# Optimization experiments

Hardware: AMD Instinct MI355X
Metric: run time of the kernel (lower is better)

## Reference

```python
import jax, jax.numpy as jnp
import numpy as np

EPS = 1e-5
NUM_HEAD = 8
HEAD_DIM = 64
SCALE = HEAD_DIM ** -0.5


def setup_inputs() -> dict:
    key = jax.random.key(0)
    ks = jax.random.split(key, 3)
    b, n, dim = 4, 2048, 512
    inner = NUM_HEAD * HEAD_DIM  # 512
    x = jax.random.normal(ks[0], (b, n, dim), dtype=jnp.float32)
    ln_w = jnp.ones((dim,), jnp.float32)
    ln_b = jnp.zeros((dim,), jnp.float32)
    qkv_w = jax.random.normal(ks[1], (3 * inner, dim), jnp.float32) * (dim ** -0.5)
    qkv_b = jnp.zeros((3 * inner,), jnp.float32)
    out_w = jax.random.normal(ks[2], (dim, inner), jnp.float32) * (inner ** -0.5)
    out_b = jnp.zeros((dim,), jnp.float32)
    return {"x": x, "ln_w": ln_w, "ln_b": ln_b, "qkv_w": qkv_w,
            "qkv_b": qkv_b, "out_w": out_w, "out_b": out_b}


def reference(x, ln_w, ln_b, qkv_w, qkv_b, out_w, out_b):
    b, n, dim = x.shape
    # Pre-norm LayerNorm
    mu = jnp.mean(x, axis=-1, keepdims=True)
    var = jnp.mean(jnp.square(x - mu), axis=-1, keepdims=True)
    xn = (x - mu) * jax.lax.rsqrt(var + EPS) * ln_w + ln_b
    # QKV projection (torch Linear: y = x @ W.T + b)
    qkv = xn @ qkv_w.T + qkv_b  # [b, n, 3*inner]
    q, k, v = jnp.split(qkv, 3, axis=-1)
    def heads(t):  # [b, n, inner] -> [b, h, n, d]
        return t.reshape(b, n, NUM_HEAD, HEAD_DIM).transpose(0, 2, 1, 3)
    q, k, v = heads(q), heads(k), heads(v)
    # Naive full attention (materializes [b, h, n, n])
    dots = jnp.einsum('bhqd,bhkd->bhqk', q, k) * SCALE
    attn = jax.nn.softmax(dots, axis=-1)
    o = jnp.einsum('bhqk,bhkd->bhqd', attn, v)
    o = o.transpose(0, 2, 1, 3).reshape(b, n, NUM_HEAD * HEAD_DIM)
    return o @ out_w.T + out_b
```

## Files before the change

kernel.cpp:

```cpp
#include <hip/hip_runtime.h>

typedef __attribute__((ext_vector_type(8))) short bf16x8;
typedef __attribute__((ext_vector_type(4))) float floatx4;
typedef __attribute__((ext_vector_type(16))) float floatx16;
typedef __attribute__((ext_vector_type(4))) unsigned int uintx4;

#define B_    4
#define N_    2048
#define DIM_  512
#define NH_   8
#define HD_   64
#define SCALE_ 0.125f
#define SL2E_ (0.125f * 1.44269504f)

__device__ __forceinline__ unsigned short f32_to_bf16(float f) {
    return (unsigned short)((__float_as_uint(f) + 0x8000u) >> 16);
}

__device__ __forceinline__ float bf16_to_f32(unsigned short u) {
    return __uint_as_float(((unsigned int)u) << 16);
}

__device__ __forceinline__ floatx4 mfma16(bf16x8 a, bf16x8 b, floatx4 c) {
    return __builtin_amdgcn_mfma_f32_16x16x32_bf16(a, b, c, 0, 0, 0);
}

__device__ __forceinline__ floatx16 mfma32(bf16x8 a, bf16x8 b, floatx16 c) {
    return __builtin_amdgcn_mfma_f32_32x32x16_bf16(a, b, c, 0, 0, 0);
}

__device__ __forceinline__ floatx4 fzero4() {
    floatx4 z = {0.f, 0.f, 0.f, 0.f};
    return z;
}

__device__ __forceinline__ floatx16 fzero16() {
    floatx16 z;
#pragma unroll
    for (int i = 0; i < 16; i++) z[i] = 0.f;
    return z;
}

__device__ __forceinline__ unsigned int cvt_pk_bf16(float lo, float hi) {
    unsigned int r;
    asm("v_cvt_pk_bf16_f32 %0, %1, %2" : "=v"(r) : "v"(lo), "v"(hi));
    return r;
}

__device__ __forceinline__ void async16(const unsigned short* g, unsigned short* l) {
    __builtin_amdgcn_global_load_lds((const __attribute__((address_space(1))) void*)g,
                                     (__attribute__((address_space(3))) void*)l,
                                     16, 0, 0);
}

__global__ __launch_bounds__(256) void ln_kernel(const float* __restrict__ x,
                                                 const float* __restrict__ w,
                                                 const float* __restrict__ b,
                                                 unsigned short* __restrict__ xn) {
    int wv = threadIdx.x >> 6;
    int lane = threadIdx.x & 63;
    int row = blockIdx.x * 4 + wv;
    const float4* xr = (const float4*)(x + (size_t)row * DIM_);
    float4 v0 = xr[lane * 2];
    float4 v1 = xr[lane * 2 + 1];
    float s  = (v0.x + v0.y + v0.z + v0.w) + (v1.x + v1.y + v1.z + v1.w);
    float sq = v0.x*v0.x + v0.y*v0.y + v0.z*v0.z + v0.w*v0.w +
               v1.x*v1.x + v1.y*v1.y + v1.z*v1.z + v1.w*v1.w;
#pragma unroll
    for (int off = 1; off < 64; off <<= 1) {
        s  += __shfl_xor(s, off, 64);
        sq += __shfl_xor(sq, off, 64);
    }
    float mu   = s * (1.f / DIM_);
    float var  = sq * (1.f / DIM_) - mu * mu;
    float rstd = rsqrtf(var + 1e-5f);
    float4 w0 = ((const float4*)w)[lane * 2];
    float4 w1 = ((const float4*)w)[lane * 2 + 1];
    float4 b0 = ((const float4*)b)[lane * 2];
    float4 b1 = ((const float4*)b)[lane * 2 + 1];
    float y[8];
    y[0] = (v0.x - mu) * rstd * w0.x + b0.x;
    y[1] = (v0.y - mu) * rstd * w0.y + b0.y;
    y[2] = (v0.z - mu) * rstd * w0.z + b0.z;
    y[3] = (v0.w - mu) * rstd * w0.w + b0.w;
    y[4] = (v1.x - mu) * rstd * w1.x + b1.x;
    y[5] = (v1.y - mu) * rstd * w1.y + b1.y;
    y[6] = (v1.z - mu) * rstd * w1.z + b1.z;
    y[7] = (v1.w - mu) * rstd * w1.w + b1.w;
    uint4 pk;
    pk.x = (unsigned int)f32_to_bf16(y[0]) | ((unsigned int)f32_to_bf16(y[1]) << 16);
    pk.y = (unsigned int)f32_to_bf16(y[2]) | ((unsigned int)f32_to_bf16(y[3]) << 16);
    pk.z = (unsigned int)f32_to_bf16(y[4]) | ((unsigned int)f32_to_bf16(y[5]) << 16);
    pk.w = (unsigned int)f32_to_bf16(y[6]) | ((unsigned int)f32_to_bf16(y[7]) << 16);
    ((uint4*)(xn + (size_t)row * DIM_))[lane] = pk;
}

__global__ __launch_bounds__(256) void cvt_kernel(const float* __restrict__ srcA, int na,
                                                  const float* __restrict__ srcB, int nb,
                                                  unsigned short* __restrict__ dstA,
                                                  unsigned short* __restrict__ dstB) {
    int idx = blockIdx.x * 256 + threadIdx.x;
    if (idx < na)            dstA[idx] = f32_to_bf16(srcA[idx]);
    else if (idx < na + nb)  dstB[idx - na] = f32_to_bf16(srcB[idx - na]);
}

#define GEMM_CORE512(A_, B_ptr, am0, bn0)                                           \
    __shared__ unsigned short Alds[2][128][32];                                     \
    __shared__ unsigned short Blds[2][128][32];                                     \
    int tid = threadIdx.x, lane = tid & 63, wid = tid >> 6;                         \
    int l15 = lane & 15, quad = lane >> 4;                                          \
    int wmloc = (wid >> 1) * 32, wnloc = (wid & 1) * 64;                            \
    int sr = lane >> 2;                                                             \
    int sc = (lane & 3) * 8;                                                        \
    int srow0 = 16 * wid;                                                           \
    floatx4 acc[2][4];                                                              \
    _Pragma("unroll")                                                               \
    for (int i = 0; i < 2; i++)                                                     \
        _Pragma("unroll")                                                           \
        for (int j = 0; j < 4; j++) acc[i][j] = fzero4();                           \
    int buf = 0;                                                                    \
    async16(A_ + (size_t)(am0 + srow0 + sr) * DIM_ + sc, &Alds[0][srow0][0]);       \
    async16(B_ptr + (size_t)(bn0 + srow0 + sr) * DIM_ + sc, &Blds[0][srow0][0]);    \
    __syncthreads();                                                                \
    for (int t = 0; t < 16; t++) {                                                  \
        if (t < 15) {                                                               \
            int k0 = (t + 1) * 32;                                                  \
            async16(A_ + (size_t)(am0 + srow0 + sr) * DIM_ + k0 + sc,               \
                    &Alds[buf ^ 1][srow0][0]);                                      \
            async16(B_ptr + (size_t)(bn0 + srow0 + sr) * DIM_ + k0 + sc,            \
                    &Blds[buf ^ 1][srow0][0]);                                      \
        }                                                                           \
        bf16x8 av[2], bv[4];                                                        \
        _Pragma("unroll")                                                           \
        for (int i = 0; i < 2; i++)                                                 \
            av[i] = *(const bf16x8*)(&Alds[buf][wmloc + 16 * i + l15][quad * 8]);   \
        _Pragma("unroll")                                                           \
        for (int j = 0; j < 4; j++)                                                 \
            bv[j] = *(const bf16x8*)(&Blds[buf][wnloc + 16 * j + l15][quad * 8]);   \
        _Pragma("unroll")                                                           \
        for (int i = 0; i < 2; i++)                                                 \
            _Pragma("unroll")                                                       \
            for (int j = 0; j < 4; j++)                                             \
                acc[i][j] = mfma16(av[i], bv[j], acc[i][j]);                        \
        __syncthreads();                                                            \
        buf ^= 1;                                                                   \
    }

__global__ __launch_bounds__(512, 6) void qkv_gemm(const unsigned short* __restrict__ A,
                                                   const unsigned short* __restrict__ Bw,
                                                   const float* __restrict__ bias,
                                                   unsigned short* __restrict__ Qh,
                                                   unsigned short* __restrict__ Kh,
                                                   unsigned short* __restrict__ Vt) {
    int am0 = blockIdx.x * 128, bn0 = blockIdx.y * 128;
    GEMM_CORE512(A, Bw, am0, bn0)

    if (bn0 >= 1024) {
        unsigned short* sc_ = &Alds[0][0][0] + wid * (16 * 40);
        int m0 = am0 + wmloc;
        int bidx = m0 >> 11;
        int t0 = m0 & 2047;
#pragma unroll
        for (int j = 0; j < 4; j++) {
            float bias_n = bias[bn0 + wnloc + 16 * j + l15];
#pragma unroll
            for (int i = 0; i < 2; i++)
#pragma unroll
                for (int r = 0; r < 4; r++)
                    sc_[l15 * 40 + 16 * i + quad * 4 + r] =
                        f32_to_bf16(acc[i][j][r] + bias_n);
            int nr = lane >> 2;
            int rem = (bn0 - 1024) + wnloc + 16 * j + nr;
            int head = rem >> 6, d = rem & 63;
            bf16x8 vv = *(const bf16x8*)(sc_ + nr * 40 + (lane & 3) * 8);
            *(bf16x8*)(Vt + ((size_t)(bidx * NH_ + head) * HD_ + d) * N_ +
                       t0 + (lane & 3) * 8) = vv;
        }
    } else {
#pragma unroll
        for (int i = 0; i < 2; i++) {
#pragma unroll
            for (int j = 0; j < 4; j++) {
                int n = bn0 + wnloc + 16 * j + l15;
                float bias_n = bias[n];
                int which = n >> 9;
                int rem = n & 511;
                int head = rem >> 6;
                int d = rem & 63;
#pragma unroll
                for (int r = 0; r < 4; r++) {
                    int m = am0 + wmloc + 16 * i + quad * 4 + r;
                    int b = m >> 11;
                    int t = m & 2047;
                    float val = acc[i][j][r] + bias_n;
                    if (which == 0) {
                        Qh[((size_t)(b * NH_ + head) * N_ + t) * HD_ + d] =
                            f32_to_bf16(val * SL2E_);
                    } else {
                        Kh[((size_t)(b * NH_ + head) * N_ + t) * HD_ + d] =
                            f32_to_bf16(val);
                    }
                }
            }
        }
    }
}

__global__ __launch_bounds__(256, 4) void out_gemm_fused(const unsigned short* __restrict__ Opart,
                                                         const float* __restrict__ lpart,
                                                         const unsigned short* __restrict__ Bw,
                                                         const float* __restrict__ bias,
                                                         float* __restrict__ out) {
    __shared__ unsigned short Alds[2][64][36];
    __shared__ unsigned short Blds[2][128][32];
    int tid = threadIdx.x, lane = tid & 63, wid = tid >> 6;
    int l15 = lane & 15, quad = lane >> 4;
    int wmloc = (wid >> 1) * 32, wnloc = (wid & 1) * 64;
    int am0 = blockIdx.x * 64, bn0 = blockIdx.y * 128;

    int arow = tid >> 2;
    int ac8 = (tid & 3) * 8;
    int token = am0 + arow;
    int bb = token >> 11;
    const size_t LSTR = (size_t)B_ * NH_ * N_;
    const size_t OSTR = (size_t)B_ * N_ * DIM_;
    const unsigned short* arow0 = Opart + (size_t)token * DIM_;
    const unsigned short* arow1 = arow0 + OSTR;

    int sr = lane >> 2;
    int sc = (lane & 3) * 8;

    floatx4 acc[2][4];
#pragma unroll
    for (int i = 0; i < 2; i++)
#pragma unroll
        for (int j = 0; j < 4; j++) acc[i][j] = fzero4();

#define STAGE_A(BUF, T)                                                         \
    {                                                                           \
        int k0 = (T) * 32;                                                      \
        int head = k0 >> 6;                                                     \
        size_t li = (size_t)(bb * NH_ + head) * N_ + (token & 2047);            \
        float l1 = lpart[li];                                                   \
        float l2 = lpart[LSTR + li];                                            \
        float inv = 1.f / (l1 + l2);                                            \
        float w1 = l1 * inv, w2 = l2 * inv;                                     \
        bf16x8 o0 = *(const bf16x8*)(arow0 + k0 + ac8);                         \
        bf16x8 o1 = *(const bf16x8*)(arow1 + k0 + ac8);                         \
        bf16x8 pk;                                                              \
        _Pragma("unroll")                                                       \
        for (int e = 0; e < 8; e++)                                             \
            pk[e] = (short)f32_to_bf16(                                         \
                w1 * bf16_to_f32((unsigned short)o0[e]) +                       \
                w2 * bf16_to_f32((unsigned short)o1[e]));                       \
        *(bf16x8*)(&Alds[BUF][arow][ac8]) = pk;                                 \
    }

#define STAGE_B(BUF, T)                                                         \
    {                                                                           \
        int k0 = (T) * 32;                                                      \
        _Pragma("unroll")                                                       \
        for (int i = 0; i < 2; i++) {                                           \
            int r0 = 32 * wid + 16 * i;                                         \
            async16(Bw + (size_t)(bn0 + r0 + sr) * DIM_ + k0 + sc,              \
                    &Blds[BUF][r0][0]);                                         \
        }                                                                       \
    }

    STAGE_B(0, 0)
    STAGE_A(0, 0)
    __syncthreads();
    int buf = 0;
    for (int t = 0; t < 16; t++) {
        if (t < 15) {
            STAGE_B(buf ^ 1, t + 1)
            STAGE_A(buf ^ 1, t + 1)
        }
        bf16x8 av[2], bv[4];
#pragma unroll
        for (int i = 0; i < 2; i++)
            av[i] = *(const bf16x8*)(&Alds[buf][wmloc + 16 * i + l15][quad * 8]);
#pragma unroll
        for (int j = 0; j < 4; j++)
            bv[j] = *(const bf16x8*)(&Blds[buf][wnloc + 16 * j + l15][quad * 8]);
#pragma unroll
        for (int i = 0; i < 2; i++)
#pragma unroll
            for (int j = 0; j < 4; j++)
                acc[i][j] = mfma16(av[i], bv[j], acc[i][j]);
        __syncthreads();
        buf ^= 1;
    }
#undef STAGE_A
#undef STAGE_B

#pragma unroll
    for (int i = 0; i < 2; i++) {
#pragma unroll
        for (int j = 0; j < 4; j++) {
            int n = bn0 + wnloc + 16 * j + l15;
            float bias_n = bias[n];
#pragma unroll
            for (int r = 0; r < 4; r++) {
                int m = am0 + wmloc + 16 * i + quad * 4 + r;
                out[(size_t)m * DIM_ + n] = acc[i][j][r] + bias_n;
            }
        }
    }
}

__global__ __launch_bounds__(256, 4) void attn_kernel(const unsigned short* __restrict__ Qh,
                                                      const unsigned short* __restrict__ Kh,
                                                      const unsigned short* __restrict__ Vtg,
                                                      unsigned short* __restrict__ Opart,
                                                      float* __restrict__ lpart) {
    int bh = blockIdx.y;
    int b = bh >> 3, head = bh & 7;
    int qt = blockIdx.x;
    int split = blockIdx.z;
    int kv0 = split << 10;
    int tid = threadIdx.x, lane = tid & 63, w = tid >> 6;
    int l31 = lane & 31, hi = lane >> 5;
    int xr = l31 & 7;

    const unsigned short* Qp = Qh + (size_t)bh * N_ * HD_;
    const unsigned short* Kg = Kh + (size_t)bh * N_ * HD_;
    const unsigned short* Vg = Vtg + (size_t)bh * HD_ * N_;

    int q0 = qt * 128 + w * 32;

    bf16x8 aQ[4];
    {
        const unsigned short* qrow = Qp + (size_t)(q0 + l31) * HD_ + hi * 8;
#pragma unroll
        for (int t = 0; t < 4; t++)
            aQ[t] = *(const bf16x8*)(qrow + 16 * t);
    }

    __shared__ unsigned short KV[2][2][64][64];
    __shared__ float l_sm[4][32];

    int srow = lane >> 3;
    int scol = ((lane & 7) ^ srow) * 8;

    const char* ptc[4];
#pragma unroll
    for (int t = 0; t < 4; t++)
        ptc[t] = (const char*)&KV[0][0][l31][(((2 * t + hi) ^ xr) * 8)];

    const unsigned short* kSrc = Kg + (size_t)(kv0 + 16 * w + srow) * HD_ + scol;
    const unsigned short* vSrc = Vg + (size_t)(16 * w + srow) * N_ + kv0 + scol;

#define STAGE_KV(BUF, IT)                                                       \
    {                                                                           \
        _Pragma("unroll")                                                       \
        for (int i = 0; i < 2; i++) {                                           \
            int r0 = 16 * w + 8 * i;                                            \
            async16(kSrc + (size_t)(IT) * 64 * HD_ + i * 8 * HD_,               \
                    &KV[BUF][0][r0][0]);                                        \
            async16(vSrc + (size_t)(IT) * 64 + i * 8 * N_,                      \
                    &KV[BUF][1][r0][0]);                                        \
        }                                                                       \
    }

    floatx16 of[2];
    of[0] = fzero16();
    of[1] = fzero16();
    float lsA = 0.f, lsB = 0.f;

#define COMPUTE(BUF)                                                            \
    {                                                                           \
        bf16x8 pa[4];                                                           \
        _Pragma("unroll")                                                       \
        for (int tau = 0; tau < 2; tau++) {                                     \
            bf16x8 kf[4];                                                       \
            _Pragma("unroll")                                                   \
            for (int t = 0; t < 4; t++)                                         \
                kf[t] = *(const bf16x8*)(ptc[t] + (BUF) * 16384 + tau * 4096);  \
            floatx16 acc = fzero16();                                           \
            __builtin_amdgcn_s_setprio(1);                                      \
            _Pragma("unroll")                                                   \
            for (int t = 0; t < 4; t++)                                         \
                acc = mfma32(kf[t], aQ[t], acc);                                \
            __builtin_amdgcn_s_setprio(0);                                      \
            float p[16];                                                        \
            _Pragma("unroll")                                                   \
            for (int r = 0; r < 16; r += 2) {                                   \
                p[r]     = __builtin_amdgcn_exp2f(acc[r]);                      \
                p[r + 1] = __builtin_amdgcn_exp2f(acc[r + 1]);                  \
                lsA += p[r];                                                    \
                lsB += p[r + 1];                                                \
            }                                                                   \
            unsigned int a0 = cvt_pk_bf16(p[0], p[1]);                          \
            unsigned int b0 = cvt_pk_bf16(p[4], p[5]);                          \
            unsigned int a1 = cvt_pk_bf16(p[2], p[3]);                          \
            unsigned int b1 = cvt_pk_bf16(p[6], p[7]);                          \
            unsigned int a2 = cvt_pk_bf16(p[8], p[9]);                          \
            unsigned int b2 = cvt_pk_bf16(p[12], p[13]);                        \
            unsigned int a3 = cvt_pk_bf16(p[10], p[11]);                        \
            unsigned int b3 = cvt_pk_bf16(p[14], p[15]);                        \
            asm("v_permlane32_swap_b32 %0, %1" : "+v"(a0), "+v"(b0));           \
            asm("v_permlane32_swap_b32 %0, %1" : "+v"(a1), "+v"(b1));           \
            asm("v_permlane32_swap_b32 %0, %1" : "+v"(a2), "+v"(b2));           \
            asm("v_permlane32_swap_b32 %0, %1" : "+v"(a3), "+v"(b3));           \
            uintx4 f0 = {a0, a1, b0, b1};                                       \
            uintx4 f1 = {a2, a3, b2, b3};                                       \
            pa[2 * tau]     = __builtin_bit_cast(bf16x8, f0);                   \
            pa[2 * tau + 1] = __builtin_bit_cast(bf16x8, f1);                   \
        }                                                                       \
        __builtin_amdgcn_s_setprio(1);                                          \
        _Pragma("unroll")                                                       \
        for (int s = 0; s < 4; s++) {                                           \
            _Pragma("unroll")                                                   \
            for (int dt = 0; dt < 2; dt++) {                                    \
                bf16x8 vf = *(const bf16x8*)(ptc[s] + (BUF) * 16384 + 8192 +    \
                                             dt * 4096);                        \
                of[dt] = mfma32(pa[s], vf, of[dt]);                             \
            }                                                                   \
        }                                                                       \
        __builtin_amdgcn_s_setprio(0);                                          \
    }

    STAGE_KV(0, 0)
    __syncthreads();

    for (int it2 = 0; it2 < 8; it2++) {
        int it = it2 * 2;
        STAGE_KV(1, it + 1)
        COMPUTE(0)
        __syncthreads();
        if (it2 < 7) STAGE_KV(0, it + 2)
        COMPUTE(1)
        __syncthreads();
    }
#undef STAGE_KV
#undef COMPUTE

    float lsum = lsA + lsB;
    lsum += __shfl_xor(lsum, 32, 64);
    if (hi == 0) {
        l_sm[w][l31] = __builtin_amdgcn_rcpf(lsum);
        lpart[(size_t)split * B_ * NH_ * N_ + (size_t)bh * N_ + q0 + l31] = lsum;
    }
    asm volatile("s_waitcnt lgkmcnt(0)" ::: "memory");

    unsigned short* Od = Opart + (size_t)split * B_ * N_ * DIM_;
#pragma unroll
    for (int r = 0; r < 16; r++) {
        int qr = (r & 3) + 8 * (r >> 2) + 4 * hi;
        float inv = l_sm[w][qr];
        int token = q0 + qr;
        size_t base = ((size_t)b * N_ + token) * DIM_ + (size_t)head * HD_;
#pragma unroll
        for (int dt = 0; dt < 2; dt++)
            Od[base + 32 * dt + l31] = f32_to_bf16(of[dt][r] * inv);
    }
}

extern "C" void kernel_launch(void* const* d_in, const int* in_sizes, int n_in,
                              void* d_out, int out_size, void* d_ws, size_t ws_size,
                              hipStream_t stream) {
    const float* x     = (const float*)d_in[0];
    const float* ln_w  = (const float*)d_in[1];
    const float* ln_b  = (const float*)d_in[2];
    const float* qkv_w = (const float*)d_in[3];
    const float* qkv_b = (const float*)d_in[4];
    const float* out_w = (const float*)d_in[5];
    const float* out_b = (const float*)d_in[6];
    float* out = (float*)d_out;

    char* ws = (char*)d_ws;
    const size_t TOK = (size_t)B_ * N_;
    unsigned short* xn    = (unsigned short*)ws;  ws += TOK * DIM_ * 2;
    unsigned short* wq_bf = (unsigned short*)ws;  ws += (size_t)3 * DIM_ * DIM_ * 2;
    unsigned short* wo_bf = (unsigned short*)ws;  ws += (size_t)DIM_ * DIM_ * 2;
    unsigned short* Qh    = (unsigned short*)ws;  ws += TOK * DIM_ * 2;
    unsigned short* Kh    = (unsigned short*)ws;  ws += TOK * DIM_ * 2;
    unsigned short* Vt    = (unsigned short*)ws;  ws += TOK * DIM_ * 2;
    unsigned short* Opart = (unsigned short*)ws;  ws += (size_t)2 * TOK * DIM_ * 2;
    float*          lpart = (float*)ws;           ws += (size_t)2 * B_ * NH_ * N_ * 4;

    const int NW = 3 * DIM_ * DIM_;
    const int NO = DIM_ * DIM_;

    ln_kernel<<<TOK / 4, 256, 0, stream>>>(x, ln_w, ln_b, xn);
    cvt_kernel<<<(NW + NO + 255) / 256, 256, 0, stream>>>(qkv_w, NW, out_w, NO, wq_bf, wo_bf);
    qkv_gemm<<<dim3(TOK / 128, (3 * DIM_) / 128), 512, 0, stream>>>(xn, wq_bf, qkv_b, Qh, Kh, Vt);
    attn_kernel<<<dim3(N_ / 128, B_ * NH_, 2), 256, 0, stream>>>(Qh, Kh, Vt, Opart, lpart);
    out_gemm_fused<<<dim3(TOK / 64, DIM_ / 128), 256, 0, stream>>>(Opart, lpart, wo_bf, out_b, out);
}
```

Before: 161.8 us.

## Fuse LayerNorm with weight conversion and double attention block query tile

```diff
diff --git a/kernel.cpp b/kernel.cpp
--- a/kernel.cpp
+++ b/kernel.cpp
@@ -53,55 +53,67 @@
                                      16, 0, 0);
 }
 
-__global__ __launch_bounds__(256) void ln_kernel(const float* __restrict__ x,
-                                                 const float* __restrict__ w,
-                                                 const float* __restrict__ b,
-                                                 unsigned short* __restrict__ xn) {
-    int wv = threadIdx.x >> 6;
-    int lane = threadIdx.x & 63;
-    int row = blockIdx.x * 4 + wv;
-    const float4* xr = (const float4*)(x + (size_t)row * DIM_);
-    float4 v0 = xr[lane * 2];
-    float4 v1 = xr[lane * 2 + 1];
-    float s  = (v0.x + v0.y + v0.z + v0.w) + (v1.x + v1.y + v1.z + v1.w);
-    float sq = v0.x*v0.x + v0.y*v0.y + v0.z*v0.z + v0.w*v0.w +
-               v1.x*v1.x + v1.y*v1.y + v1.z*v1.z + v1.w*v1.w;
-#pragma unroll
-    for (int off = 1; off < 64; off <<= 1) {
-        s  += __shfl_xor(s, off, 64);
-        sq += __shfl_xor(sq, off, 64);
-    }
-    float mu   = s * (1.f / DIM_);
-    float var  = sq * (1.f / DIM_) - mu * mu;
-    float rstd = rsqrtf(var + 1e-5f);
-    float4 w0 = ((const float4*)w)[lane * 2];
-    float4 w1 = ((const float4*)w)[lane * 2 + 1];
-    float4 b0 = ((const float4*)b)[lane * 2];
-    float4 b1 = ((const float4*)b)[lane * 2 + 1];
-    float y[8];
-    y[0] = (v0.x - mu) * rstd * w0.x + b0.x;
-    y[1] = (v0.y - mu) * rstd * w0.y + b0.y;
-    y[2] = (v0.z - mu) * rstd * w0.z + b0.z;
-    y[3] = (v0.w - mu) * rstd * w0.w + b0.w;
-    y[4] = (v1.x - mu) * rstd * w1.x + b1.x;
-    y[5] = (v1.y - mu) * rstd * w1.y + b1.y;
-    y[6] = (v1.z - mu) * rstd * w1.z + b1.z;
-    y[7] = (v1.w - mu) * rstd * w1.w + b1.w;
-    uint4 pk;
-    pk.x = (unsigned int)f32_to_bf16(y[0]) | ((unsigned int)f32_to_bf16(y[1]) << 16);
-    pk.y = (unsigned int)f32_to_bf16(y[2]) | ((unsigned int)f32_to_bf16(y[3]) << 16);
-    pk.z = (unsigned int)f32_to_bf16(y[4]) | ((unsigned int)f32_to_bf16(y[5]) << 16);
-    pk.w = (unsigned int)f32_to_bf16(y[6]) | ((unsigned int)f32_to_bf16(y[7]) << 16);
-    ((uint4*)(xn + (size_t)row * DIM_))[lane] = pk;
-}
-
-__global__ __launch_bounds__(256) void cvt_kernel(const float* __restrict__ srcA, int na,
-                                                  const float* __restrict__ srcB, int nb,
-                                                  unsigned short* __restrict__ dstA,
-                                                  unsigned short* __restrict__ dstB) {
-    int idx = blockIdx.x * 256 + threadIdx.x;
-    if (idx < na)            dstA[idx] = f32_to_bf16(srcA[idx]);
-    else if (idx < na + nb)  dstB[idx - na] = f32_to_bf16(srcB[idx - na]);
+__global__ __launch_bounds__(256) void ln_cvt_kernel(const float* __restrict__ x,
+                                                     const float* __restrict__ w,
+                                                     const float* __restrict__ b,
+                                                     unsigned short* __restrict__ xn,
+                                                     const float* __restrict__ srcA,
+                                                     const float* __restrict__ srcB,
+                                                     unsigned short* __restrict__ dstA,
+                                                     unsigned short* __restrict__ dstB) {
+    const int NWQ = 3 * DIM_ * DIM_;
+    if (blockIdx.x < 2048) {
+        int wv = threadIdx.x >> 6;
+        int lane = threadIdx.x & 63;
+        int row = blockIdx.x * 4 + wv;
+        const float4* xr = (const float4*)(x + (size_t)row * DIM_);
+        float4 v0 = xr[lane * 2];
+        float4 v1 = xr[lane * 2 + 1];
+        float s  = (v0.x + v0.y + v0.z + v0.w) + (v1.x + v1.y + v1.z + v1.w);
+        float sq = v0.x*v0.x + v0.y*v0.y + v0.z*v0.z + v0.w*v0.w +
+                   v1.x*v1.x + v1.y*v1.y + v1.z*v1.z + v1.w*v1.w;
+#pragma unroll
+        for (int off = 1; off < 64; off <<= 1) {
+            s  += __shfl_xor(s, off, 64);
+            sq += __shfl_xor(sq, off, 64);
+        }
+        float mu   = s * (1.f / DIM_);
+        float var  = sq * (1.f / DIM_) - mu * mu;
+        float rstd = rsqrtf(var + 1e-5f);
+        float4 w0 = ((const float4*)w)[lane * 2];
+        float4 w1 = ((const float4*)w)[lane * 2 + 1];
+        float4 b0 = ((const float4*)b)[lane * 2];
+        float4 b1 = ((const float4*)b)[lane * 2 + 1];
+        float y[8];
+        y[0] = (v0.x - mu) * rstd * w0.x + b0.x;
+        y[1] = (v0.y - mu) * rstd * w0.y + b0.y;
+        y[2] = (v0.z - mu) * rstd * w0.z + b0.z;
+        y[3] = (v0.w - mu) * rstd * w0.w + b0.w;
+        y[4] = (v1.x - mu) * rstd * w1.x + b1.x;
+        y[5] = (v1.y - mu) * rstd * w1.y + b1.y;
+        y[6] = (v1.z - mu) * rstd * w1.z + b1.z;
+        y[7] = (v1.w - mu) * rstd * w1.w + b1.w;
+        uint4 pk;
+        pk.x = (unsigned int)f32_to_bf16(y[0]) | ((unsigned int)f32_to_bf16(y[1]) << 16);
+        pk.y = (unsigned int)f32_to_bf16(y[2]) | ((unsigned int)f32_to_bf16(y[3]) << 16);
+        pk.z = (unsigned int)f32_to_bf16(y[4]) | ((unsigned int)f32_to_bf16(y[5]) << 16);
+        pk.w = (unsigned int)f32_to_bf16(y[6]) | ((unsigned int)f32_to_bf16(y[7]) << 16);
+        ((uint4*)(xn + (size_t)row * DIM_))[lane] = pk;
+    } else {
+        int e0 = ((blockIdx.x - 2048) * 256 + threadIdx.x) * 8;
+        const float* src;
+        unsigned short* dst;
+        if (e0 < NWQ) { src = srcA + e0; dst = dstA + e0; }
+        else          { src = srcB + (e0 - NWQ); dst = dstB + (e0 - NWQ); }
+        float4 u0 = ((const float4*)src)[0];
+        float4 u1 = ((const float4*)src)[1];
+        uint4 pk;
+        pk.x = (unsigned int)f32_to_bf16(u0.x) | ((unsigned int)f32_to_bf16(u0.y) << 16);
+        pk.y = (unsigned int)f32_to_bf16(u0.z) | ((unsigned int)f32_to_bf16(u0.w) << 16);
+        pk.z = (unsigned int)f32_to_bf16(u1.x) | ((unsigned int)f32_to_bf16(u1.y) << 16);
+        pk.w = (unsigned int)f32_to_bf16(u1.z) | ((unsigned int)f32_to_bf16(u1.w) << 16);
+        *(uint4*)dst = pk;
+    }
 }
 
 #define GEMM_CORE512(A_, B_ptr, am0, bn0)                                           \
@@ -309,7 +321,7 @@
     }
 }
 
-__global__ __launch_bounds__(256, 4) void attn_kernel(const unsigned short* __restrict__ Qh,
+__global__ __launch_bounds__(512, 4) void attn_kernel(const unsigned short* __restrict__ Qh,
                                                       const unsigned short* __restrict__ Kh,
                                                       const unsigned short* __restrict__ Vtg,
                                                       unsigned short* __restrict__ Opart,
@@ -327,7 +339,7 @@
     const unsigned short* Kg = Kh + (size_t)bh * N_ * HD_;
     const unsigned short* Vg = Vtg + (size_t)bh * HD_ * N_;
 
-    int q0 = qt * 128 + w * 32;
+    int q0 = qt * 256 + w * 32;
 
     bf16x8 aQ[4];
     {
@@ -338,7 +350,7 @@
     }
 
     __shared__ unsigned short KV[2][2][64][64];
-    __shared__ float l_sm[4][32];
+    __shared__ float l_sm[8][32];
 
     int srow = lane >> 3;
     int scol = ((lane & 7) ^ srow) * 8;
@@ -348,19 +360,13 @@
     for (int t = 0; t < 4; t++)
         ptc[t] = (const char*)&KV[0][0][l31][(((2 * t + hi) ^ xr) * 8)];
 
-    const unsigned short* kSrc = Kg + (size_t)(kv0 + 16 * w + srow) * HD_ + scol;
-    const unsigned short* vSrc = Vg + (size_t)(16 * w + srow) * N_ + kv0 + scol;
+    const unsigned short* kSrc = Kg + (size_t)(kv0 + 8 * w + srow) * HD_ + scol;
+    const unsigned short* vSrc = Vg + (size_t)(8 * w + srow) * N_ + kv0 + scol;
 
 #define STAGE_KV(BUF, IT)                                                       \
     {                                                                           \
-        _Pragma("unroll")                                                       \
-        for (int i = 0; i < 2; i++) {                                           \
-            int r0 = 16 * w + 8 * i;                                            \
-            async16(kSrc + (size_t)(IT) * 64 * HD_ + i * 8 * HD_,               \
-                    &KV[BUF][0][r0][0]);                                        \
-            async16(vSrc + (size_t)(IT) * 64 + i * 8 * N_,                      \
-                    &KV[BUF][1][r0][0]);                                        \
-        }                                                                       \
+        async16(kSrc + (size_t)(IT) * 64 * HD_, &KV[BUF][0][8 * w][0]);         \
+        async16(vSrc + (size_t)(IT) * 64, &KV[BUF][1][8 * w][0]);               \
     }
 
     floatx16 of[2];
@@ -480,12 +486,9 @@
     unsigned short* Opart = (unsigned short*)ws;  ws += (size_t)2 * TOK * DIM_ * 2;
     float*          lpart = (float*)ws;           ws += (size_t)2 * B_ * NH_ * N_ * 4;
 
-    const int NW = 3 * DIM_ * DIM_;
-    const int NO = DIM_ * DIM_;
-
-    ln_kernel<<<TOK / 4, 256, 0, stream>>>(x, ln_w, ln_b, xn);
-    cvt_kernel<<<(NW + NO + 255) / 256, 256, 0, stream>>>(qkv_w, NW, out_w, NO, wq_bf, wo_bf);
+    ln_cvt_kernel<<<2048 + 512, 256, 0, stream>>>(x, ln_w, ln_b, xn,
+                                                  qkv_w, out_w, wq_bf, wo_bf);
     qkv_gemm<<<dim3(TOK / 128, (3 * DIM_) / 128), 512, 0, stream>>>(xn, wq_bf, qkv_b, Qh, Kh, Vt);
-    attn_kernel<<<dim3(N_ / 128, B_ * NH_, 2), 256, 0, stream>>>(Qh, Kh, Vt, Opart, lpart);
+    attn_kernel<<<dim3(N_ / 256, B_ * NH_, 2), 512, 0, stream>>>(Qh, Kh, Vt, Opart, lpart);
     out_gemm_fused<<<dim3(TOK / 64, DIM_ / 128), 256, 0, stream>>>(Opart, lpart, wo_bf, out_b, out);
 }
```

After: 153.5 us. -5.1%, faster.
